# Kernel optimization log

Hardware: AMD Instinct MI355X
Metric: run time of the kernel (lower is better)

Reference implementation:

```python
import jax, jax.numpy as jnp
import numpy as np

SHIFT = 1  # original module picks random(+1/-1) at init; fixed to +1 for determinism


def setup_inputs() -> dict:
    key = jax.random.key(0)
    k1, k2, k3 = jax.random.split(key, 3)
    x = jax.random.normal(k1, (1024, 1792, 14), dtype=jnp.float32)
    w1 = jax.random.normal(k2, (256, 2), dtype=jnp.float32)      # weights[0]
    w2 = jax.random.normal(k3, (128, 3, 256), dtype=jnp.float32)  # weights[1]
    return {"x": x, "w1": w1, "w2": w2}


def reference(x, w1, w2):
    m = 1024
    # Channels 1792 split as j(128) * l(14); H = 14. unfold((3,1), pad=(1,0)) is an
    # im2col over H with 3 taps; torch orders the unfolded channel dim as c*3+k,
    # so reshape (1024, 128, 14, 3, 14) puts taps k before spatial n -> permute to mjlnk.
    x4 = x.reshape(m, 128, 14, 14)                       # (m, j, l, h)
    xp = jnp.pad(x4, ((0, 0), (0, 0), (0, 0), (1, 1)))   # pad H by 1 each side
    win = jnp.stack([xp[..., 0:14], xp[..., 1:15], xp[..., 2:16]], axis=-1)  # (m,j,l,n,k)
    t4 = jnp.einsum('mjlnk,jki->mlni', win, w2)          # (1024, 14, 14, 256)
    t5 = jnp.einsum('mabj,ji->mabji', t4, w1)            # (1024, 14, 14, 256, 2) outer product
    t6 = jnp.roll(t5, SHIFT, axis=1)
    t6 = t6.transpose(0, 2, 3, 1, 4).reshape(m, 14, 256, 28)
    t6 = jnp.roll(t6, SHIFT, axis=3)
    t6 = t6.reshape(m, 14, 256, 14, 2).sum(axis=4)       # pairwise sum
    return t6.transpose(0, 2, 3, 1)                      # (1024, 256, 14, 14)
```

## Files before the change

### kernel.cpp

```cpp
#include <hip/hip_runtime.h>

typedef __bf16 bf16x8 __attribute__((ext_vector_type(8)));
typedef unsigned short u16x8 __attribute__((ext_vector_type(8)));
typedef float f32x4 __attribute__((ext_vector_type(4)));

__device__ __forceinline__ unsigned short f2bf(float f) {
    unsigned u = __builtin_bit_cast(unsigned, f);
    u += 0x7FFFu + ((u >> 16) & 1u);
    return (unsigned short)(u >> 16);
}
__device__ __forceinline__ float bflo(unsigned w) {
    return __builtin_bit_cast(float, w << 16);
}
__device__ __forceinline__ float bfhi(unsigned w) {
    return __builtin_bit_cast(float, w & 0xFFFF0000u);
}

__global__ void prep_w2(const float* __restrict__ w2, unsigned short* __restrict__ w2t) {
    int idx = blockIdx.x * 256 + threadIdx.x;
    if (idx < 128 * 3 * 256) {
        int i  = idx % 256;
        int jk = idx / 256;
        int j2 = jk / 3, k = jk % 3;
        w2t[i * 384 + k * 128 + j2] = f2bf(w2[idx]);
    }
}

__device__ __forceinline__ void load14(const float* __restrict__ p, bool odd, float v[14]) {
    if (odd) {
        const float2 a  = *(const float2*)(p);
        const float4 q0 = *(const float4*)(p + 2);
        const float4 q1 = *(const float4*)(p + 6);
        const float4 q2 = *(const float4*)(p + 10);
        v[0]=a.x;  v[1]=a.y;
        v[2]=q0.x; v[3]=q0.y; v[4]=q0.z;  v[5]=q0.w;
        v[6]=q1.x; v[7]=q1.y; v[8]=q1.z;  v[9]=q1.w;
        v[10]=q2.x; v[11]=q2.y; v[12]=q2.z; v[13]=q2.w;
    } else {
        const float4 q0 = *(const float4*)(p);
        const float4 q1 = *(const float4*)(p + 4);
        const float4 q2 = *(const float4*)(p + 8);
        const float2 a  = *(const float2*)(p + 12);
        v[0]=q0.x; v[1]=q0.y; v[2]=q0.z;  v[3]=q0.w;
        v[4]=q1.x; v[5]=q1.y; v[6]=q1.z;  v[7]=q1.w;
        v[8]=q2.x; v[9]=q2.y; v[10]=q2.z; v[11]=q2.w;
        v[12]=a.x; v[13]=a.y;
    }
}

__global__ __launch_bounds__(256, 2) void fused_conv_outer3(
    const float* __restrict__ x, const float* __restrict__ w1,
    const unsigned short* __restrict__ w2t, float* __restrict__ out)
{
    __shared__ alignas(16) unsigned short xlds[128 * 136];
    __shared__ alignas(16) unsigned short cb[4 * 112 * 34];

    const int m    = blockIdx.x >> 1;
    const int half = blockIdx.x & 1;
    const int tid  = threadIdx.x;
    const int wave = tid >> 6;
    const int lane = tid & 63;
    const int c16  = lane & 15;
    const int kgrp = lane >> 4;

    for (int i = tid; i < 1088; i += 256) {
        const int zr   = i / 68;
        const int w    = i - zr * 68;
        const int lrow = (zr >> 1) * 16 + ((zr & 1) ? 15 : 0);
        *(unsigned*)&xlds[lrow * 136 + w * 2] = 0;
    }

    {
        const float* xm = x + (size_t)m * 25088;
        const int j2a = 2 * lane;
#pragma unroll
        for (int t = 0; t < 2; ++t) {
            const int li = wave * 2 + t;
            const int gl = half ? (6 + li) : (li < 7 ? li : 13);
            float va[14], vb[14];
            const float* b0 = xm + (size_t)j2a * 196 + gl * 14;
            load14(b0,       (gl & 1) != 0, va);
            load14(b0 + 196, (gl & 1) != 0, vb);
            unsigned short* dst = &xlds[(li * 16 + 1) * 136 + j2a];
#pragma unroll
            for (int h = 0; h < 14; ++h) {
                unsigned pk = (unsigned)f2bf(va[h]) | ((unsigned)f2bf(vb[h]) << 16);
                *(unsigned*)&dst[h * 136] = pk;
            }
        }
    }
    __syncthreads();

    unsigned short* cbw = &cb[wave * (112 * 34)];
    float* outm = out + (size_t)m * 50176;

#pragma unroll 1
    for (int np = 0; np < 2; ++np) {
        const int colbase = wave * 64 + np * 32;

        bf16x8 B0[12], B1[12];
        {
            const unsigned short* bp0 = w2t + (size_t)(colbase + c16) * 384 + kgrp * 8;
            const unsigned short* bp1 = bp0 + 16 * 384;
#pragma unroll
            for (int k = 0; k < 12; ++k) {
                B0[k] = __builtin_bit_cast(bf16x8, *(const u16x8*)(bp0 + k * 32));
                B1[k] = __builtin_bit_cast(bf16x8, *(const u16x8*)(bp1 + k * 32));
            }
        }

#pragma unroll 1
        for (int mt = 0; mt < 7; ++mt) {
            const int r0 = mt * 16 + c16;
            const int li = r0 / 14;
            const int rb = r0 + 2 * li;

            bf16x8 Af[12];
#pragma unroll
            for (int k = 0; k < 12; ++k) {
                const int tap = k >> 2;
                Af[k] = __builtin_bit_cast(bf16x8,
                    *(const u16x8*)&xlds[(rb + tap) * 136 + (k & 3) * 32 + kgrp * 8]);
            }

            f32x4 a0 = {0.f, 0.f, 0.f, 0.f};
            f32x4 a1 = {0.f, 0.f, 0.f, 0.f};
#pragma unroll
            for (int k = 0; k < 12; ++k) {
                a0 = __builtin_amdgcn_mfma_f32_16x16x32_bf16(Af[k], B0[k], a0, 0, 0, 0);
                a1 = __builtin_amdgcn_mfma_f32_16x16x32_bf16(Af[k], B1[k], a1, 0, 0, 0);
            }

            const int rrb = mt * 16 + kgrp * 4;
#pragma unroll
            for (int j = 0; j < 4; ++j) {
                cbw[(rrb + j) * 34 + c16]      = f2bf(a0[j]);
                cbw[(rrb + j) * 34 + 16 + c16] = f2bf(a1[j]);
            }
        }

        asm volatile("s_waitcnt lgkmcnt(0)" ::: "memory");

        float* op = outm + (size_t)colbase * 196;
#pragma unroll
        for (int it = 0; it < 2; ++it) {
            const int e   = it * 64 + lane;
            const bool ok = (e < 98);
            const int ec  = ok ? e : 97;
            const int ci  = ec / 14;
            const int n2  = ec - ci * 14;
            int li1, li2, o;
            if (half) { li1 = ci + 1; li2 = ci;            o = e + 112 - (ci == 6 ? 196 : 0); }
            else      { li1 = ci;     li2 = (ci + 7) & 7;  o = e + 14; }
            const int r1o = (li1 * 14 + n2) * 34;
            const int r2o = (li2 * 14 + n2) * 34;
#pragma unroll
            for (int cp = 0; cp < 16; ++cp) {
                const float4 wv = *(const float4*)(w1 + (colbase + 2 * cp) * 2);
                const unsigned A = *(const unsigned*)&cbw[r1o + 2 * cp];
                const unsigned B = *(const unsigned*)&cbw[r2o + 2 * cp];
                if (ok) {
                    op[(2 * cp) * 196 + o]     = wv.x * bflo(A) + wv.y * bflo(B);
                    op[(2 * cp + 1) * 196 + o] = wv.z * bfhi(A) + wv.w * bfhi(B);
                }
            }
        }

        asm volatile("" ::: "memory");
    }
}

extern "C" void kernel_launch(void* const* d_in, const int* in_sizes, int n_in,
                              void* d_out, int out_size, void* d_ws, size_t ws_size,
                              hipStream_t stream) {
    const float* x  = (const float*)d_in[0];
    const float* w1 = (const float*)d_in[1];
    const float* w2 = (const float*)d_in[2];
    float* out = (float*)d_out;
    unsigned short* w2t = (unsigned short*)d_ws;

    prep_w2<<<384, 256, 0, stream>>>(w2, w2t);
    fused_conv_outer3<<<2048, 256, 0, stream>>>(x, w1, w2t, out);
}
```

Baseline: 368.1 us.

## Prefetch weight fragments early, pack column pairs, overlap next B load with epilogue

Weight B fragments for the first column half are now loaded before the x staging, so they overlap the global x loads. The second half's fragments are prefetched after the first GEMM and before the first epilogue. Column assignment is interleaved (2*c16, 2*c16+1) so each lane packs both MFMA outputs into one 32-bit LDS word, halving LDS stores and epilogue reads. The mt loop is fully unrolled. The cost is higher register pressure from the unrolling and early prefetch under launch_bounds(256,2).

New measurement: 377.0 us. +2.4%, slower.

```diff
diff --git a/kernel.cpp b/kernel.cpp
--- a/kernel.cpp
+++ b/kernel.cpp
@@ -48,12 +48,12 @@
     }
 }
 
-__global__ __launch_bounds__(256, 2) void fused_conv_outer3(
+__global__ __launch_bounds__(256, 2) void fused_conv_outer4(
     const float* __restrict__ x, const float* __restrict__ w1,
     const unsigned short* __restrict__ w2t, float* __restrict__ out)
 {
     __shared__ alignas(16) unsigned short xlds[128 * 136];
-    __shared__ alignas(16) unsigned short cb[4 * 112 * 34];
+    __shared__ alignas(16) unsigned cb32[4 * 112 * 17];
 
     const int m    = blockIdx.x >> 1;
     const int half = blockIdx.x & 1;
@@ -62,6 +62,19 @@
     const int lane = tid & 63;
     const int c16  = lane & 15;
     const int kgrp = lane >> 4;
+
+    const int colbase0 = wave * 64;
+    const int colbase1 = wave * 64 + 32;
+
+    bf16x8 B0[12], B1[12];
+    {
+        const unsigned short* bp0 = w2t + (size_t)(colbase0 + 2 * c16) * 384 + kgrp * 8;
+#pragma unroll
+        for (int k = 0; k < 12; ++k) {
+            B0[k] = __builtin_bit_cast(bf16x8, *(const u16x8*)(bp0 + k * 32));
+            B1[k] = __builtin_bit_cast(bf16x8, *(const u16x8*)(bp0 + 384 + k * 32));
+        }
+    }
 
     for (int i = tid; i < 1088; i += 256) {
         const int zr   = i / 68;
@@ -91,25 +104,11 @@
     }
     __syncthreads();
 
-    unsigned short* cbw = &cb[wave * (112 * 34)];
+    unsigned* cbw = &cb32[wave * (112 * 17)];
     float* outm = out + (size_t)m * 50176;
 
-#pragma unroll 1
-    for (int np = 0; np < 2; ++np) {
-        const int colbase = wave * 64 + np * 32;
-
-        bf16x8 B0[12], B1[12];
-        {
-            const unsigned short* bp0 = w2t + (size_t)(colbase + c16) * 384 + kgrp * 8;
-            const unsigned short* bp1 = bp0 + 16 * 384;
+    auto gemm = [&](const bf16x8* Bl, const bf16x8* Br) {
 #pragma unroll
-            for (int k = 0; k < 12; ++k) {
-                B0[k] = __builtin_bit_cast(bf16x8, *(const u16x8*)(bp0 + k * 32));
-                B1[k] = __builtin_bit_cast(bf16x8, *(const u16x8*)(bp1 + k * 32));
-            }
-        }
-
-#pragma unroll 1
         for (int mt = 0; mt < 7; ++mt) {
             const int r0 = mt * 16 + c16;
             const int li = r0 / 14;
@@ -127,20 +126,19 @@
             f32x4 a1 = {0.f, 0.f, 0.f, 0.f};
 #pragma unroll
             for (int k = 0; k < 12; ++k) {
-                a0 = __builtin_amdgcn_mfma_f32_16x16x32_bf16(Af[k], B0[k], a0, 0, 0, 0);
-                a1 = __builtin_amdgcn_mfma_f32_16x16x32_bf16(Af[k], B1[k], a1, 0, 0, 0);
+                a0 = __builtin_amdgcn_mfma_f32_16x16x32_bf16(Af[k], Bl[k], a0, 0, 0, 0);
+                a1 = __builtin_amdgcn_mfma_f32_16x16x32_bf16(Af[k], Br[k], a1, 0, 0, 0);
             }
 
             const int rrb = mt * 16 + kgrp * 4;
 #pragma unroll
-            for (int j = 0; j < 4; ++j) {
-                cbw[(rrb + j) * 34 + c16]      = f2bf(a0[j]);
-                cbw[(rrb + j) * 34 + 16 + c16] = f2bf(a1[j]);
-            }
+            for (int j = 0; j < 4; ++j)
+                cbw[(rrb + j) * 17 + c16] =
+                    (unsigned)f2bf(a0[j]) | ((unsigned)f2bf(a1[j]) << 16);
         }
+    };
 
-        asm volatile("s_waitcnt lgkmcnt(0)" ::: "memory");
-
+    auto epilogue = [&](int colbase) {
         float* op = outm + (size_t)colbase * 196;
 #pragma unroll
         for (int it = 0; it < 2; ++it) {
@@ -152,22 +150,39 @@
             int li1, li2, o;
             if (half) { li1 = ci + 1; li2 = ci;            o = e + 112 - (ci == 6 ? 196 : 0); }
             else      { li1 = ci;     li2 = (ci + 7) & 7;  o = e + 14; }
-            const int r1o = (li1 * 14 + n2) * 34;
-            const int r2o = (li2 * 14 + n2) * 34;
+            const int r1o = (li1 * 14 + n2) * 17;
+            const int r2o = (li2 * 14 + n2) * 17;
 #pragma unroll
             for (int cp = 0; cp < 16; ++cp) {
                 const float4 wv = *(const float4*)(w1 + (colbase + 2 * cp) * 2);
-                const unsigned A = *(const unsigned*)&cbw[r1o + 2 * cp];
-                const unsigned B = *(const unsigned*)&cbw[r2o + 2 * cp];
+                const unsigned A = cbw[r1o + cp];
+                const unsigned B = cbw[r2o + cp];
                 if (ok) {
                     op[(2 * cp) * 196 + o]     = wv.x * bflo(A) + wv.y * bflo(B);
                     op[(2 * cp + 1) * 196 + o] = wv.z * bfhi(A) + wv.w * bfhi(B);
                 }
             }
         }
+    };
 
-        asm volatile("" ::: "memory");
+    gemm(B0, B1);
+
+    {
+        const unsigned short* bp0 = w2t + (size_t)(colbase1 + 2 * c16) * 384 + kgrp * 8;
+#pragma unroll
+        for (int k = 0; k < 12; ++k) {
+            B0[k] = __builtin_bit_cast(bf16x8, *(const u16x8*)(bp0 + k * 32));
+            B1[k] = __builtin_bit_cast(bf16x8, *(const u16x8*)(bp0 + 384 + k * 32));
+        }
     }
+
+    asm volatile("s_waitcnt lgkmcnt(0)" ::: "memory");
+    epilogue(colbase0);
+    asm volatile("" ::: "memory");
+
+    gemm(B0, B1);
+    asm volatile("s_waitcnt lgkmcnt(0)" ::: "memory");
+    epilogue(colbase1);
 }
 
 extern "C" void kernel_launch(void* const* d_in, const int* in_sizes, int n_in,
@@ -180,5 +195,5 @@
     unsigned short* w2t = (unsigned short*)d_ws;
 
     prep_w2<<<384, 256, 0, stream>>>(w2, w2t);
-    fused_conv_outer3<<<2048, 256, 0, stream>>>(x, w1, w2t, out);
+    fused_conv_outer4<<<2048, 256, 0, stream>>>(x, w1, w2t, out);
 }
```
